# Optimization experiments

Hardware: AMD Instinct MI355X
Metric: run time of the kernel (lower is better)

## Reference

```python
import jax, jax.numpy as jnp
import numpy as np

B1, B2, D = 8192, 8192, 128


def _cdist(d1, d2):
    # L2 distance matrix via the |a|^2 + |b|^2 - 2ab expansion (GEMM-dominant).
    d1_sq = jnp.sum(d1 * d1, axis=1, keepdims=True)          # (B1, 1)
    d2_sq = jnp.sum(d2 * d2, axis=1, keepdims=True)          # (B2, 1)
    dm = d1_sq + d2_sq.T - 2.0 * (d1 @ d2.T)                 # (B1, B2)
    return jnp.sqrt(jnp.clip(dm, 0.0))


def setup_inputs() -> dict:
    key = jax.random.key(0)
    k1, k2 = jax.random.split(key)
    desc1 = jax.random.normal(k1, (B1, D), dtype=jnp.float32)
    desc2 = jax.random.normal(k2, (B2, D), dtype=jnp.float32)
    return {"desc1": desc1, "desc2": desc2}


def reference(desc1, desc2):
    # DescriptorMatcher(match_mode='nn'): nearest neighbor in desc2 for each desc1.
    dm = _cdist(desc1, desc2)                                # (B1, B2)
    idxs_in_2 = jnp.argmin(dm, axis=1)                       # (B1,)
    match_dists = jnp.take_along_axis(dm, idxs_in_2[:, None], axis=1)  # (B1, 1)
    idxs_in_1 = jnp.arange(dm.shape[0], dtype=jnp.int64 if jax.config.jax_enable_x64 else jnp.int32)
    matches_idxs = jnp.stack([idxs_in_1, idxs_in_2.astype(idxs_in_1.dtype)], axis=1)  # (B1, 2)
    return match_dists, matches_idxs
```

## Files before the change

### kernel.cpp

```cpp
#include <hip/hip_runtime.h>
#include <cstdint>

#define NB1 8192
#define NB2 8192
#define DDIM 128
#define KROW 256
#define NSTEP 12

using half8   = __attribute__((ext_vector_type(8))) _Float16;
using half4   = __attribute__((ext_vector_type(4))) _Float16;
using float4v = __attribute__((ext_vector_type(4))) float;

typedef __attribute__((address_space(3))) void       lds_void;
typedef const __attribute__((address_space(1))) void glb_void;

__device__ inline unsigned long long packkey(float v, int j) {
  unsigned u = __float_as_uint(v);
  u = (u & 0x80000000u) ? ~u : (u | 0x80000000u);
  return ((unsigned long long)u << 32) | (unsigned)j;
}

__device__ __forceinline__ int a_src(int kt) { return (kt < 8) ? kt : kt - 8; }
__device__ __forceinline__ int b_src(int kt) { return (kt < 4) ? kt : kt - 4; }

__global__ __launch_bounds__(256) void convert_kernel(
    const float* __restrict__ d1, const float* __restrict__ d2,
    _Float16* __restrict__ A2, _Float16* __restrict__ B2,
    float* __restrict__ asq, float* __restrict__ bsq,
    unsigned long long* __restrict__ packed) {
  int gid  = blockIdx.x * 256 + threadIdx.x;
  int wv   = gid >> 6;
  int lane = gid & 63;
  int rowc = 2 * wv + (lane >> 5);
  bool isA = rowc < NB1;
  const float* src = isA ? d1 : d2;
  int row = isA ? rowc : rowc - NB1;
  int k4  = (lane & 31) * 4;

  float4 v = *(const float4*)&src[row * DDIM + k4];
  _Float16 h0 = (_Float16)v.x, h1 = (_Float16)v.y;
  _Float16 h2 = (_Float16)v.z, h3 = (_Float16)v.w;
  half4 hh = {h0, h1, h2, h3};
  half4 ll = {(_Float16)(v.x - (float)h0), (_Float16)(v.y - (float)h1),
              (_Float16)(v.z - (float)h2), (_Float16)(v.w - (float)h3)};

  _Float16* dst = (isA ? A2 : B2) + (size_t)row * KROW;
  *(half4*)&dst[k4]       = hh;
  *(half4*)&dst[128 + k4] = ll;

  float s = v.x * v.x + v.y * v.y + v.z * v.z + v.w * v.w;
  #pragma unroll
  for (int off = 16; off > 0; off >>= 1) s += __shfl_xor(s, off, 64);
  if ((lane & 31) == 0) (isA ? asq : bsq)[row] = s;

  if (gid < NB1) packed[gid] = 0xFFFFFFFFFFFFFFFFull;
}

__global__ __launch_bounds__(512, 2) void mfma_match_kernel(
    const _Float16* __restrict__ A2, const _Float16* __restrict__ B2,
    const float* __restrict__ bsq, unsigned long long* __restrict__ packed) {
  __shared__ unsigned long long smem[16384];
  _Float16* S = (_Float16*)smem;

  const int t    = threadIdx.x;
  const int lane = t & 63;
  const int wid  = t >> 6;
  const int wm   = wid >> 1;
  const int wn   = wid & 1;
  const int lx   = lane & 15, q = lane >> 4;

  const int id  = blockIdx.x;
  const int xcd = id & 7, kk = id >> 3;
  const int bx = (xcd & 1) * 16 + (kk & 15);
  const int by = (xcd >> 1) * 8 + (kk >> 4);
  const int row0 = bx * 256, col0 = by * 256;

  const int rstg  = t >> 2;
  const int cslot = t & 3;

  float4v acc[4][8];
  #pragma unroll
  for (int m = 0; m < 4; ++m)
    #pragma unroll
    for (int c = 0; c < 8; ++c) acc[m][c] = (float4v){0.f, 0.f, 0.f, 0.f};

  const int jc0 = col0 + wn * 128 + lx;
  float bq[8];
  #pragma unroll
  for (int c = 0; c < 8; ++c) bq[c] = bsq[jc0 + 16 * c];

  auto stage = [&](int kt, int buf) {
    const int koA = a_src(kt) * 32, koB = b_src(kt) * 32;
    #pragma unroll
    for (int call = 0; call < 2; ++call) {
      const int R  = call * 128 + rstg;
      const int cc = (cslot - (R >> 1)) & 3;
      const _Float16* ga = A2 + (size_t)(row0 + R) * KROW + koA + cc * 8;
      __builtin_amdgcn_global_load_lds((glb_void*)ga,
          (lds_void*)(S + buf * 16384 + call * 4096 + wid * 512), 16, 0, 0);
      const _Float16* gb = B2 + (size_t)(col0 + R) * KROW + koB + cc * 8;
      __builtin_amdgcn_global_load_lds((glb_void*)gb,
          (lds_void*)(S + buf * 16384 + 8192 + call * 4096 + wid * 512), 16, 0, 0);
    }
  };

  const int sw = ((q + (lx >> 1)) & 3) * 8;

  auto compute = [&](int buf) {
    const _Float16* Ab = S + buf * 16384;
    const _Float16* Bb = Ab + 8192;
    half8 af[4], bf[8];
    #pragma unroll
    for (int m = 0; m < 4; ++m)
      af[m] = *(const half8*)&Ab[(wm * 64 + 16 * m + lx) * 32 + sw];
    #pragma unroll
    for (int c = 0; c < 8; ++c)
      bf[c] = *(const half8*)&Bb[(wn * 128 + 16 * c + lx) * 32 + sw];
    __builtin_amdgcn_s_setprio(1);
    #pragma unroll
    for (int m = 0; m < 4; ++m)
      #pragma unroll
      for (int c = 0; c < 8; ++c)
        acc[m][c] = __builtin_amdgcn_mfma_f32_16x16x32_f16(
            af[m], bf[c], acc[m][c], 0, 0, 0);
    __builtin_amdgcn_s_setprio(0);
  };

  stage(0, 0); stage(1, 1); stage(2, 2);

#define STEP(K, N)                                                    \
  do {                                                                \
    asm volatile("s_waitcnt vmcnt(" #N ")" ::: "memory");             \
    __builtin_amdgcn_s_barrier();                                     \
    asm volatile("" ::: "memory");                                    \
    if constexpr ((K) + 3 < NSTEP) stage((K) + 3, ((K) + 3) & 3);     \
    compute((K) & 3);                                                 \
  } while (0)

  STEP(0, 8);  STEP(1, 8);  STEP(2, 8);  STEP(3, 8);
  STEP(4, 8);  STEP(5, 8);  STEP(6, 8);  STEP(7, 8);
  STEP(8, 8);  STEP(9, 8);  STEP(10, 4); STEP(11, 0);
#undef STEP

  __syncthreads();
  #pragma unroll
  for (int m = 0; m < 4; ++m) {
    #pragma unroll
    for (int reg = 0; reg < 4; ++reg) {
      float bv = 1e30f; int bj = 0;
      #pragma unroll
      for (int c = 0; c < 8; ++c) {
        float val = fmaf(-2.f, acc[m][c][reg], bq[c]);
        if (val < bv) { bv = val; bj = jc0 + 16 * c; }
      }
      const int mrow = wm * 64 + 16 * m + 4 * q + reg;
      smem[mrow * 33 + wn * 16 + lx] = packkey(bv, bj);
    }
  }
  __syncthreads();
  if (t < 256) {
    unsigned long long best = ~0ull;
    #pragma unroll
    for (int c = 0; c < 32; ++c) {
      unsigned long long kx = smem[t * 33 + ((2 * t + c) & 31)];
      if (kx < best) best = kx;
    }
    atomicMin(&packed[row0 + t], best);
  }
}

__global__ __launch_bounds__(256) void out_kernel(
    const unsigned long long* __restrict__ packed,
    const float* __restrict__ asq, float* __restrict__ out) {
  int r = blockIdx.x * 256 + threadIdx.x;
  unsigned long long best = packed[r];
  unsigned u = (unsigned)(best >> 32);
  u = (u & 0x80000000u) ? (u & 0x7fffffffu) : ~u;
  float val  = __uint_as_float(u);
  float dist = sqrtf(fmaxf(asq[r] + val, 0.f));
  int j = (int)(unsigned)(best & 0xffffffffu);
  out[r]               = dist;
  out[NB1 + 2 * r]     = (float)r;
  out[NB1 + 2 * r + 1] = (float)j;
}

extern "C" void kernel_launch(void* const* d_in, const int* in_sizes, int n_in,
                              void* d_out, int out_size, void* d_ws, size_t ws_size,
                              hipStream_t stream) {
  const float* d1 = (const float*)d_in[0];
  const float* d2 = (const float*)d_in[1];
  float* out = (float*)d_out;

  char* w = (char*)d_ws;
  float* asq = (float*)w;
  float* bsq = (float*)(w + 32768);
  _Float16* A2 = (_Float16*)(w + 65536);
  _Float16* B2 = (_Float16*)(w + 65536 + 4194304);
  unsigned long long* packed =
      (unsigned long long*)(w + 65536 + 2 * 4194304);

  convert_kernel<<<(NB1 + NB2) / 8, 256, 0, stream>>>(
      d1, d2, A2, B2, asq, bsq, packed);

  mfma_match_kernel<<<(NB1 / 256) * (NB2 / 256), 512, 0, stream>>>(
      A2, B2, bsq, packed);

  out_kernel<<<NB1 / 256, 256, 0, stream>>>(packed, asq, out);
}
```

Measured before the change: 117.8 us.

## Split each K-step into two half-phases interleaving LDS reads, staging and MFMA

Restructures the main GEMM loop so each K step runs in two phases. Each phase issues half the B-fragment LDS reads and half the global-to-LDS staging, then a block of 16 MFMAs, with extra barriers between phases. The aim is to overlap LDS reads and global loads with MFMA work, ping-pong style, and to cut register pressure by holding only 4 B fragments. It adds four barriers per step, which may cost more than the overlap gains.

```diff
diff --git a/kernel.cpp b/kernel.cpp
--- a/kernel.cpp
+++ b/kernel.cpp
@@ -89,57 +89,73 @@
   #pragma unroll
   for (int c = 0; c < 8; ++c) bq[c] = bsq[jc0 + 16 * c];
 
-  auto stage = [&](int kt, int buf) {
+  auto stage_half = [&](int kt, int buf, int call) {
     const int koA = a_src(kt) * 32, koB = b_src(kt) * 32;
-    #pragma unroll
-    for (int call = 0; call < 2; ++call) {
-      const int R  = call * 128 + rstg;
-      const int cc = (cslot - (R >> 1)) & 3;
-      const _Float16* ga = A2 + (size_t)(row0 + R) * KROW + koA + cc * 8;
-      __builtin_amdgcn_global_load_lds((glb_void*)ga,
-          (lds_void*)(S + buf * 16384 + call * 4096 + wid * 512), 16, 0, 0);
-      const _Float16* gb = B2 + (size_t)(col0 + R) * KROW + koB + cc * 8;
-      __builtin_amdgcn_global_load_lds((glb_void*)gb,
-          (lds_void*)(S + buf * 16384 + 8192 + call * 4096 + wid * 512), 16, 0, 0);
-    }
+    const int R  = call * 128 + rstg;
+    const int cc = (cslot - (R >> 1)) & 3;
+    const _Float16* ga = A2 + (size_t)(row0 + R) * KROW + koA + cc * 8;
+    __builtin_amdgcn_global_load_lds((glb_void*)ga,
+        (lds_void*)(S + buf * 16384 + call * 4096 + wid * 512), 16, 0, 0);
+    const _Float16* gb = B2 + (size_t)(col0 + R) * KROW + koB + cc * 8;
+    __builtin_amdgcn_global_load_lds((glb_void*)gb,
+        (lds_void*)(S + buf * 16384 + 8192 + call * 4096 + wid * 512), 16, 0, 0);
   };
 
   const int sw = ((q + (lx >> 1)) & 3) * 8;
 
-  auto compute = [&](int buf) {
-    const _Float16* Ab = S + buf * 16384;
-    const _Float16* Bb = Ab + 8192;
-    half8 af[4], bf[8];
-    #pragma unroll
-    for (int m = 0; m < 4; ++m)
-      af[m] = *(const half8*)&Ab[(wm * 64 + 16 * m + lx) * 32 + sw];
-    #pragma unroll
-    for (int c = 0; c < 8; ++c)
-      bf[c] = *(const half8*)&Bb[(wn * 128 + 16 * c + lx) * 32 + sw];
-    __builtin_amdgcn_s_setprio(1);
-    #pragma unroll
-    for (int m = 0; m < 4; ++m)
-      #pragma unroll
-      for (int c = 0; c < 8; ++c)
-        acc[m][c] = __builtin_amdgcn_mfma_f32_16x16x32_f16(
-            af[m], bf[c], acc[m][c], 0, 0, 0);
-    __builtin_amdgcn_s_setprio(0);
-  };
-
-  stage(0, 0); stage(1, 1); stage(2, 2);
-
-#define STEP(K, N)                                                    \
-  do {                                                                \
-    asm volatile("s_waitcnt vmcnt(" #N ")" ::: "memory");             \
-    __builtin_amdgcn_s_barrier();                                     \
-    asm volatile("" ::: "memory");                                    \
-    if constexpr ((K) + 3 < NSTEP) stage((K) + 3, ((K) + 3) & 3);     \
-    compute((K) & 3);                                                 \
+  half8 af[4], bf[4];
+
+  stage_half(0, 0, 0); stage_half(0, 0, 1);
+  stage_half(1, 1, 0); stage_half(1, 1, 1);
+  stage_half(2, 2, 0); stage_half(2, 2, 1);
+  asm volatile("s_waitcnt vmcnt(8)" ::: "memory");
+  __builtin_amdgcn_s_barrier();
+
+#define STEP(K, NV, DOSTAGE)                                                  \
+  do {                                                                        \
+    { const _Float16* Ab = S + ((K) & 3) * 16384;                             \
+      const _Float16* Bb = Ab + 8192;                                         \
+      _Pragma("unroll")                                                       \
+      for (int m = 0; m < 4; ++m)                                             \
+        af[m] = *(const half8*)&Ab[(wm * 64 + 16 * m + lx) * 32 + sw];        \
+      _Pragma("unroll")                                                       \
+      for (int c = 0; c < 4; ++c)                                             \
+        bf[c] = *(const half8*)&Bb[(wn * 128 + 16 * c + lx) * 32 + sw]; }     \
+    if constexpr (DOSTAGE) stage_half((K) + 3, ((K) + 3) & 3, 0);             \
+    __builtin_amdgcn_s_barrier();                                             \
+    asm volatile("s_waitcnt lgkmcnt(0)" ::: "memory");                        \
+    __builtin_amdgcn_s_setprio(1);                                            \
+    _Pragma("unroll")                                                         \
+    for (int m = 0; m < 4; ++m)                                               \
+      _Pragma("unroll")                                                       \
+      for (int c = 0; c < 4; ++c)                                             \
+        acc[m][c] = __builtin_amdgcn_mfma_f32_16x16x32_f16(                   \
+            af[m], bf[c], acc[m][c], 0, 0, 0);                                \
+    __builtin_amdgcn_s_setprio(0);                                            \
+    __builtin_amdgcn_s_barrier();                                             \
+    { const _Float16* Bb = S + ((K) & 3) * 16384 + 8192;                      \
+      _Pragma("unroll")                                                       \
+      for (int c = 0; c < 4; ++c)                                             \
+        bf[c] = *(const half8*)&Bb[(wn * 128 + 64 + 16 * c + lx) * 32 + sw]; }\
+    if constexpr (DOSTAGE) stage_half((K) + 3, ((K) + 3) & 3, 1);             \
+    asm volatile("s_waitcnt vmcnt(" #NV ")" ::: "memory");                    \
+    __builtin_amdgcn_s_barrier();                                             \
+    asm volatile("s_waitcnt lgkmcnt(0)" ::: "memory");                        \
+    __builtin_amdgcn_s_setprio(1);                                            \
+    _Pragma("unroll")                                                         \
+    for (int m = 0; m < 4; ++m)                                               \
+      _Pragma("unroll")                                                       \
+      for (int c = 0; c < 4; ++c)                                             \
+        acc[m][4 + c] = __builtin_amdgcn_mfma_f32_16x16x32_f16(               \
+            af[m], bf[c], acc[m][4 + c], 0, 0, 0);                            \
+    __builtin_amdgcn_s_setprio(0);                                            \
+    __builtin_amdgcn_s_barrier();                                             \
   } while (0)
 
-  STEP(0, 8);  STEP(1, 8);  STEP(2, 8);  STEP(3, 8);
-  STEP(4, 8);  STEP(5, 8);  STEP(6, 8);  STEP(7, 8);
-  STEP(8, 8);  STEP(9, 8);  STEP(10, 4); STEP(11, 0);
+  STEP(0, 8, true);  STEP(1, 8, true);  STEP(2, 8, true);
+  STEP(3, 8, true);  STEP(4, 8, true);  STEP(5, 8, true);
+  STEP(6, 8, true);  STEP(7, 8, true);  STEP(8, 8, true);
+  STEP(9, 4, false); STEP(10, 0, false); STEP(11, 0, false);
 #undef STEP
 
   __syncthreads();
```

Result: slower. 121.1 us (+2.8%).

## Switch GEMM tile to 32x32x16 MFMA with shuffle-merged argmin epilogue

Applied to the files above, without the earlier changes.

Replaces the 16x16x32 f16 MFMA instructions with 32x32x16 ones, so each wave computes 2x4 tiles of 32x32 using two k-substeps per 32-wide LDS chunk. This cuts the LDS fragment loads per MFMA and the instruction count. The epilogue is reworked for the 32x32 accumulator layout, with a cross-lane shuffle merging half-wave candidates before writing to shared memory. LDS read swizzle offsets are recomputed for the new lane mapping, which risks bank conflicts if the mapping is wrong.

```diff
diff --git a/kernel.cpp b/kernel.cpp
--- a/kernel.cpp
+++ b/kernel.cpp
@@ -7,9 +7,9 @@
 #define KROW 256
 #define NSTEP 12
 
-using half8   = __attribute__((ext_vector_type(8))) _Float16;
-using half4   = __attribute__((ext_vector_type(4))) _Float16;
-using float4v = __attribute__((ext_vector_type(4))) float;
+using half8    = __attribute__((ext_vector_type(8))) _Float16;
+using half4    = __attribute__((ext_vector_type(4))) _Float16;
+using float16v = __attribute__((ext_vector_type(16))) float;
 
 typedef __attribute__((address_space(3))) void       lds_void;
 typedef const __attribute__((address_space(1))) void glb_void;
@@ -67,7 +67,9 @@
   const int wid  = t >> 6;
   const int wm   = wid >> 1;
   const int wn   = wid & 1;
-  const int lx   = lane & 15, q = lane >> 4;
+  const int r31  = lane & 31;
+  const int q2   = lane >> 5;
+  const int rsw  = (r31 >> 1) & 3;
 
   const int id  = blockIdx.x;
   const int xcd = id & 7, kk = id >> 3;
@@ -78,16 +80,18 @@
   const int rstg  = t >> 2;
   const int cslot = t & 3;
 
-  float4v acc[4][8];
-  #pragma unroll
-  for (int m = 0; m < 4; ++m)
-    #pragma unroll
-    for (int c = 0; c < 8; ++c) acc[m][c] = (float4v){0.f, 0.f, 0.f, 0.f};
-
-  const int jc0 = col0 + wn * 128 + lx;
-  float bq[8];
-  #pragma unroll
-  for (int c = 0; c < 8; ++c) bq[c] = bsq[jc0 + 16 * c];
+  float16v acc[2][4];
+  #pragma unroll
+  for (int mt = 0; mt < 2; ++mt)
+    #pragma unroll
+    for (int nt = 0; nt < 4; ++nt)
+      #pragma unroll
+      for (int x = 0; x < 16; ++x) acc[mt][nt][x] = 0.f;
+
+  const int jc0 = col0 + wn * 128 + r31;
+  float bq[4];
+  #pragma unroll
+  for (int nt = 0; nt < 4; ++nt) bq[nt] = bsq[jc0 + 32 * nt];
 
   auto stage = [&](int kt, int buf) {
     const int koA = a_src(kt) * 32, koB = b_src(kt) * 32;
@@ -104,25 +108,29 @@
     }
   };
 
-  const int sw = ((q + (lx >> 1)) & 3) * 8;
-
   auto compute = [&](int buf) {
     const _Float16* Ab = S + buf * 16384;
     const _Float16* Bb = Ab + 8192;
-    half8 af[4], bf[8];
-    #pragma unroll
-    for (int m = 0; m < 4; ++m)
-      af[m] = *(const half8*)&Ab[(wm * 64 + 16 * m + lx) * 32 + sw];
-    #pragma unroll
-    for (int c = 0; c < 8; ++c)
-      bf[c] = *(const half8*)&Bb[(wn * 128 + 16 * c + lx) * 32 + sw];
+    half8 af[2][2], bf[2][4];
+    #pragma unroll
+    for (int ks = 0; ks < 2; ++ks) {
+      const int sl = ((ks * 2 + q2 + rsw) & 3) * 8;
+      #pragma unroll
+      for (int mt = 0; mt < 2; ++mt)
+        af[ks][mt] = *(const half8*)&Ab[(wm * 64 + mt * 32 + r31) * 32 + sl];
+      #pragma unroll
+      for (int nt = 0; nt < 4; ++nt)
+        bf[ks][nt] = *(const half8*)&Bb[(wn * 128 + nt * 32 + r31) * 32 + sl];
+    }
     __builtin_amdgcn_s_setprio(1);
     #pragma unroll
-    for (int m = 0; m < 4; ++m)
-      #pragma unroll
-      for (int c = 0; c < 8; ++c)
-        acc[m][c] = __builtin_amdgcn_mfma_f32_16x16x32_f16(
-            af[m], bf[c], acc[m][c], 0, 0, 0);
+    for (int ks = 0; ks < 2; ++ks)
+      #pragma unroll
+      for (int mt = 0; mt < 2; ++mt)
+        #pragma unroll
+        for (int nt = 0; nt < 4; ++nt)
+          acc[mt][nt] = __builtin_amdgcn_mfma_f32_32x32x16_f16(
+              af[ks][mt], bf[ks][nt], acc[mt][nt], 0, 0, 0);
     __builtin_amdgcn_s_setprio(0);
   };
 
@@ -144,17 +152,23 @@
 
   __syncthreads();
   #pragma unroll
-  for (int m = 0; m < 4; ++m) {
-    #pragma unroll
-    for (int reg = 0; reg < 4; ++reg) {
+  for (int mt = 0; mt < 2; ++mt) {
+    #pragma unroll
+    for (int reg = 0; reg < 16; ++reg) {
       float bv = 1e30f; int bj = 0;
       #pragma unroll
-      for (int c = 0; c < 8; ++c) {
-        float val = fmaf(-2.f, acc[m][c][reg], bq[c]);
-        if (val < bv) { bv = val; bj = jc0 + 16 * c; }
+      for (int nt = 0; nt < 4; ++nt) {
+        float val = fmaf(-2.f, acc[mt][nt][reg], bq[nt]);
+        if (val < bv) { bv = val; bj = jc0 + 32 * nt; }
       }
-      const int mrow = wm * 64 + 16 * m + 4 * q + reg;
-      smem[mrow * 33 + wn * 16 + lx] = packkey(bv, bj);
+      unsigned long long key = packkey(bv, bj);
+      unsigned long long oth = __shfl_xor(key, 16, 64);
+      if (oth < key) key = oth;
+      if ((lane & 16) == 0) {
+        const int mrow =
+            wm * 64 + mt * 32 + (reg & 3) + 8 * (reg >> 2) + 4 * q2;
+        smem[mrow * 33 + wn * 16 + (lane & 15)] = key;
+      }
     }
   }
   __syncthreads();
```

Measured after the change: 136.2 us. 15.7% more time.

## Shrink match tile to 256x128 with triple buffering for higher occupancy

Applied to the files above, without the earlier changes.

Halves the column tile of the distance/argmin kernel from 256 to 128, which halves the accumulator registers per wave and doubles the grid. LDS use drops from 4 to 3 pipeline buffers and launch bounds rise to 4 blocks per CU, aiming to hide latency through more resident waves. The trade-off is more global/LDS traffic per FLOP from reloading A tiles for twice as many column blocks, more atomicMin traffic, and a shallower prefetch depth.

```diff
diff --git a/kernel.cpp b/kernel.cpp
--- a/kernel.cpp
+++ b/kernel.cpp
@@ -56,10 +56,10 @@
   if (gid < NB1) packed[gid] = 0xFFFFFFFFFFFFFFFFull;
 }
 
-__global__ __launch_bounds__(512, 2) void mfma_match_kernel(
+__global__ __launch_bounds__(512, 4) void mfma_match_kernel(
     const _Float16* __restrict__ A2, const _Float16* __restrict__ B2,
     const float* __restrict__ bsq, unsigned long long* __restrict__ packed) {
-  __shared__ unsigned long long smem[16384];
+  __shared__ unsigned long long smem[9216];
   _Float16* S = (_Float16*)smem;
 
   const int t    = threadIdx.x;
@@ -72,88 +72,90 @@
   const int id  = blockIdx.x;
   const int xcd = id & 7, kk = id >> 3;
   const int bx = (xcd & 1) * 16 + (kk & 15);
-  const int by = (xcd >> 1) * 8 + (kk >> 4);
-  const int row0 = bx * 256, col0 = by * 256;
+  const int by = (xcd >> 1) * 16 + (kk >> 4);
+  const int row0 = bx * 256, col0 = by * 128;
 
   const int rstg  = t >> 2;
   const int cslot = t & 3;
 
-  float4v acc[4][8];
-  #pragma unroll
-  for (int m = 0; m < 4; ++m)
-    #pragma unroll
-    for (int c = 0; c < 8; ++c) acc[m][c] = (float4v){0.f, 0.f, 0.f, 0.f};
-
-  const int jc0 = col0 + wn * 128 + lx;
-  float bq[8];
-  #pragma unroll
-  for (int c = 0; c < 8; ++c) bq[c] = bsq[jc0 + 16 * c];
+  float4v acc[4][4];
+  #pragma unroll
+  for (int r = 0; r < 4; ++r)
+    #pragma unroll
+    for (int c = 0; c < 4; ++c) acc[r][c] = (float4v){0.f, 0.f, 0.f, 0.f};
+
+  float bq[4]; int jc[4];
+  #pragma unroll
+  for (int c = 0; c < 4; ++c) {
+    jc[c] = col0 + wn * 64 + 16 * c + lx;
+    bq[c] = bsq[jc[c]];
+  }
 
   auto stage = [&](int kt, int buf) {
     const int koA = a_src(kt) * 32, koB = b_src(kt) * 32;
+    const int cc0 = (cslot - (rstg >> 1)) & 3;
     #pragma unroll
     for (int call = 0; call < 2; ++call) {
-      const int R  = call * 128 + rstg;
-      const int cc = (cslot - (R >> 1)) & 3;
-      const _Float16* ga = A2 + (size_t)(row0 + R) * KROW + koA + cc * 8;
+      const _Float16* ga =
+          A2 + (size_t)(row0 + call * 128 + rstg) * KROW + koA + cc0 * 8;
       __builtin_amdgcn_global_load_lds((glb_void*)ga,
-          (lds_void*)(S + buf * 16384 + call * 4096 + wid * 512), 16, 0, 0);
-      const _Float16* gb = B2 + (size_t)(col0 + R) * KROW + koB + cc * 8;
-      __builtin_amdgcn_global_load_lds((glb_void*)gb,
-          (lds_void*)(S + buf * 16384 + 8192 + call * 4096 + wid * 512), 16, 0, 0);
+          (lds_void*)(S + buf * 12288 + call * 4096 + wid * 512), 16, 0, 0);
     }
+    const _Float16* gb = B2 + (size_t)(col0 + rstg) * KROW + koB + cc0 * 8;
+    __builtin_amdgcn_global_load_lds((glb_void*)gb,
+        (lds_void*)(S + buf * 12288 + 8192 + wid * 512), 16, 0, 0);
   };
 
   const int sw = ((q + (lx >> 1)) & 3) * 8;
 
   auto compute = [&](int buf) {
-    const _Float16* Ab = S + buf * 16384;
+    const _Float16* Ab = S + buf * 12288;
     const _Float16* Bb = Ab + 8192;
-    half8 af[4], bf[8];
-    #pragma unroll
-    for (int m = 0; m < 4; ++m)
-      af[m] = *(const half8*)&Ab[(wm * 64 + 16 * m + lx) * 32 + sw];
-    #pragma unroll
-    for (int c = 0; c < 8; ++c)
-      bf[c] = *(const half8*)&Bb[(wn * 128 + 16 * c + lx) * 32 + sw];
+    half8 af[4], bf[4];
+    #pragma unroll
+    for (int r = 0; r < 4; ++r)
+      af[r] = *(const half8*)&Ab[(wm * 64 + 16 * r + lx) * 32 + sw];
+    #pragma unroll
+    for (int c = 0; c < 4; ++c)
+      bf[c] = *(const half8*)&Bb[(wn * 64 + 16 * c + lx) * 32 + sw];
     __builtin_amdgcn_s_setprio(1);
     #pragma unroll
-    for (int m = 0; m < 4; ++m)
+    for (int r = 0; r < 4; ++r)
       #pragma unroll
-      for (int c = 0; c < 8; ++c)
-        acc[m][c] = __builtin_amdgcn_mfma_f32_16x16x32_f16(
-            af[m], bf[c], acc[m][c], 0, 0, 0);
+      for (int c = 0; c < 4; ++c)
+        acc[r][c] = __builtin_amdgcn_mfma_f32_16x16x32_f16(
+            af[r], bf[c], acc[r][c], 0, 0, 0);
     __builtin_amdgcn_s_setprio(0);
   };
 
-  stage(0, 0); stage(1, 1); stage(2, 2);
+  stage(0, 0); stage(1, 1);
 
 #define STEP(K, N)                                                    \
   do {                                                                \
     asm volatile("s_waitcnt vmcnt(" #N ")" ::: "memory");             \
     __builtin_amdgcn_s_barrier();                                     \
     asm volatile("" ::: "memory");                                    \
-    if constexpr ((K) + 3 < NSTEP) stage((K) + 3, ((K) + 3) & 3);     \
-    compute((K) & 3);                                                 \
+    if constexpr ((K) + 2 < NSTEP) stage((K) + 2, ((K) + 2) % 3);     \
+    compute((K) % 3);                                                 \
   } while (0)
 
-  STEP(0, 8);  STEP(1, 8);  STEP(2, 8);  STEP(3, 8);
-  STEP(4, 8);  STEP(5, 8);  STEP(6, 8);  STEP(7, 8);
-  STEP(8, 8);  STEP(9, 8);  STEP(10, 4); STEP(11, 0);
+  STEP(0, 3);  STEP(1, 3);  STEP(2, 3);  STEP(3, 3);
+  STEP(4, 3);  STEP(5, 3);  STEP(6, 3);  STEP(7, 3);
+  STEP(8, 3);  STEP(9, 3);  STEP(10, 3); STEP(11, 0);
 #undef STEP
 
   __syncthreads();
   #pragma unroll
-  for (int m = 0; m < 4; ++m) {
+  for (int r = 0; r < 4; ++r) {
     #pragma unroll
     for (int reg = 0; reg < 4; ++reg) {
       float bv = 1e30f; int bj = 0;
       #pragma unroll
-      for (int c = 0; c < 8; ++c) {
-        float val = fmaf(-2.f, acc[m][c][reg], bq[c]);
-        if (val < bv) { bv = val; bj = jc0 + 16 * c; }
+      for (int c = 0; c < 4; ++c) {
+        float val = fmaf(-2.f, acc[r][c][reg], bq[c]);
+        if (val < bv) { bv = val; bj = jc[c]; }
       }
-      const int mrow = wm * 64 + 16 * m + 4 * q + reg;
+      const int mrow = wm * 64 + 16 * r + 4 * q + reg;
       smem[mrow * 33 + wn * 16 + lx] = packkey(bv, bj);
     }
   }
@@ -202,7 +204,7 @@
   convert_kernel<<<(NB1 + NB2) / 8, 256, 0, stream>>>(
       d1, d2, A2, B2, asq, bsq, packed);
 
-  mfma_match_kernel<<<(NB1 / 256) * (NB2 / 256), 512, 0, stream>>>(
+  mfma_match_kernel<<<(NB1 / 256) * (NB2 / 128), 512, 0, stream>>>(
       A2, B2, bsq, packed);
 
   out_kernel<<<NB1 / 256, 256, 0, stream>>>(packed, asq, out);
```

After: 122.7 us. 1.04x slower.
